# Kernel tuning notes

Hardware: AMD Instinct MI355X
Metric: run time of the kernel (lower is better)

## Reference

```python
import jax, jax.numpy as jnp
import numpy as np

BIN_SIZE = 500      # bin_size from __init__
K = 5               # num_neighbors
DIST_MULT = 0.1
MAX_NUM_BINS = 200


def setup_inputs() -> dict:
    key = jax.random.key(0)
    k1, k2 = jax.random.split(key)
    points = jax.random.normal(k1, (2, 5000, 64), dtype=jnp.float32)
    # codebook_random_rotations: [n_features, max_num_bins // 2]
    rotations = jax.random.normal(k2, (64, MAX_NUM_BINS // 2), dtype=jnp.float32)
    return {"points": points, "rotations": rotations}


def reference(points, rotations):
    """Dense equivalent of the batched tf.SparseTensor output [B, N, N].

    tf.sparse.add sums duplicate (src, dst) entries, which scatter-add
    reproduces exactly.
    """
    B, N, F = points.shape
    nbins = N // BIN_SIZE

    # LSH projection: use first nbins//2 rotation columns, mirror with -mul.
    mul = jnp.einsum('bnf,fh->bnh', points, rotations[:, : nbins // 2])
    cmul = jnp.concatenate([mul, -mul], axis=-1)          # [B, N, nbins]
    bin_idx = jnp.argmax(cmul, axis=-1)                   # [B, N]
    # split_indices_to_bins: stable argsort of bin assignment, reshape to bins
    bins_split = jnp.argsort(bin_idx, axis=-1, stable=True).reshape(B, nbins, BIN_SIZE)

    # gather points into bins: [B, nbins, BIN_SIZE, F]
    parts = jnp.take_along_axis(points, bins_split.reshape(B, N, 1), axis=1)
    parts = parts.reshape(B, nbins, BIN_SIZE, F)

    # pairwise_dist within each bin
    na = jnp.sum(parts * parts, axis=-1)                  # [B, nbins, bs]
    gram = jnp.einsum('bgif,bgjf->bgij', parts, parts)    # [B, nbins, bs, bs]
    dm = jnp.sqrt(jnp.maximum(na[..., :, None] - 2.0 * gram + na[..., None, :], 1e-6))
    aff = jnp.exp(-DIST_MULT * dm)                        # [B, nbins, bs, bs]

    # top-k neighbors per point within its bin
    vals, idx = jax.lax.top_k(aff, K)                     # [B, nbins, bs, K]

    # map local bin indices back to global point indices
    dst = jax.vmap(jax.vmap(lambda b, i: b[i]))(bins_split, idx)   # [B, nbins, bs, K]
    src = jnp.broadcast_to(bins_split[..., None], dst.shape)
    b_ix = jnp.broadcast_to(jnp.arange(B)[:, None, None, None], dst.shape)

    # scatter-add (duplicates summed, as in repeated tf.sparse.add)
    out = jnp.zeros((B, N, N), dtype=points.dtype)
    out = out.at[b_ix, src, dst].add(vals)
    return out
```

## Files before the change

### kernel.cpp

```cpp
#include <hip/hip_runtime.h>
#include <cfloat>
#include <cstddef>

#define NBATCH 2
#define NPTS   5000
#define NF     64
#define NB     10
#define BINSZ  500
#define TOPK   5
#define ROTCOLS 100

#define NCB    8
#define CBS    64
#define NCAND  (NCB * TOPK)
#define NCOMP  (NBATCH * NB * NCB)
#define NZERO  1888
#define OUT4   (NBATCH * NPTS * NPTS / 4)

__global__ __launch_bounds__(256) void bin_norm_k(const float* __restrict__ pts,
                                                  const float* __restrict__ rot,
                                                  int* __restrict__ bin_idx,
                                                  float* __restrict__ na) {
    __shared__ float srot[NF * 5];
    const int t = threadIdx.x;
    for (int i = t; i < NF * 5; i += 256) {
        int f = i / 5, h = i - 5 * f;
        srot[i] = rot[f * ROTCOLS + h];
    }
    __syncthreads();

    int pt   = blockIdx.x * 4 + (t >> 6);
    int lane = t & 63;
    float p  = pts[(size_t)pt * NF + lane];
    float nn = p * p;
    float c0 = p * srot[lane * 5 + 0];
    float c1 = p * srot[lane * 5 + 1];
    float c2 = p * srot[lane * 5 + 2];
    float c3 = p * srot[lane * 5 + 3];
    float c4 = p * srot[lane * 5 + 4];
    #pragma unroll
    for (int off = 32; off > 0; off >>= 1) {
        nn += __shfl_xor(nn, off);
        c0 += __shfl_xor(c0, off);
        c1 += __shfl_xor(c1, off);
        c2 += __shfl_xor(c2, off);
        c3 += __shfl_xor(c3, off);
        c4 += __shfl_xor(c4, off);
    }
    if (lane == 0) {
        float c[5] = {c0, c1, c2, c3, c4};
        float bv = c[0]; int bi = 0;
        #pragma unroll
        for (int h = 1; h < 5; ++h) if (c[h] > bv) { bv = c[h]; bi = h; }
        #pragma unroll
        for (int h = 0; h < 5; ++h) if (-c[h] > bv) { bv = -c[h]; bi = h + 5; }
        bin_idx[pt] = bi;
        na[pt] = nn;
    }
}

__global__ __launch_bounds__(256) void sort_k(const int* __restrict__ bin_idx,
                                              int* __restrict__ order) {
    const int b = blockIdx.x;
    const int t = threadIdx.x;
    const int w = t >> 6, lane = t & 63;
    __shared__ int sh_bin[NPTS];
    __shared__ int sh_hist[256][NB];
    __shared__ int sh_part[NB][16];
    __shared__ int sh_tot[NB + 1];

    for (int i = t; i < NPTS; i += 256) sh_bin[i] = bin_idx[b * NPTS + i];
    #pragma unroll
    for (int h = 0; h < NB; ++h) sh_hist[t][h] = 0;
    __syncthreads();

    const int CH = (NPTS + 255) / 256;
    const int i0 = t * CH;
    const int i1 = (i0 + CH < NPTS) ? (i0 + CH) : NPTS;
    for (int i = i0; i < i1; ++i) sh_hist[t][sh_bin[i]]++;
    __syncthreads();

    if (t < NB * 16) {
        int h = t >> 4, s = t & 15;
        int sum = 0;
        #pragma unroll
        for (int k = 0; k < 16; ++k) sum += sh_hist[s * 16 + k][h];
        sh_part[h][s] = sum;
    }
    __syncthreads();
    if (t < NB) {
        int tot = 0;
        #pragma unroll
        for (int s = 0; s < 16; ++s) tot += sh_part[t][s];
        sh_tot[t + 1] = tot;
    }
    __syncthreads();
    if (t == 0) {
        sh_tot[0] = 0;
        for (int h = 1; h <= NB; ++h) sh_tot[h] += sh_tot[h - 1];
    }
    __syncthreads();

    for (int h = w; h < NB; h += 4) {
        int base = lane * 4;
        int v0 = sh_hist[base + 0][h];
        int v1 = sh_hist[base + 1][h];
        int v2 = sh_hist[base + 2][h];
        int v3 = sh_hist[base + 3][h];
        int lt = v0 + v1 + v2 + v3;
        int x = lt;
        #pragma unroll
        for (int off = 1; off < 64; off <<= 1) {
            int y = __shfl_up(x, off);
            if (lane >= off) x += y;
        }
        int excl = x - lt + sh_tot[h];
        sh_hist[base + 0][h] = excl;
        sh_hist[base + 1][h] = excl + v0;
        sh_hist[base + 2][h] = excl + v0 + v1;
        sh_hist[base + 3][h] = excl + v0 + v1 + v2;
    }
    __syncthreads();

    for (int i = i0; i < i1; ++i) {
        int h = sh_bin[i];
        order[b * NPTS + sh_hist[t][h]++] = i;
    }
}

__global__ __launch_bounds__(256) void pair_zero_k(const float* __restrict__ pts,
                                                   const float* __restrict__ na,
                                                   const int* __restrict__ order,
                                                   float* __restrict__ wv,
                                                   int* __restrict__ wd,
                                                   float* __restrict__ out) {
    const int bx  = blockIdx.x;
    const int tid = threadIdx.x;

    if (bx >= NCOMP) {
        const int z = bx - NCOMP;
        const int chunk = (OUT4 + NZERO - 1) / NZERO;
        const size_t base = (size_t)z * chunk;
        size_t end = base + chunk; if (end > (size_t)OUT4) end = OUT4;
        float4* o4 = (float4*)out;
        const float4 z4 = make_float4(0.f, 0.f, 0.f, 0.f);
        for (size_t i = base + tid; i < end; i += 256) o4[i] = z4;
        return;
    }

    const int g   = bx / NCB;
    const int cb  = bx - g * NCB;
    const int b   = g / NB;
    const int grp = g - b * NB;
    const int c0  = cb * CBS;
    const int ncols = (c0 + CBS <= BINSZ) ? CBS : (BINSZ - c0);

    __shared__ float sh_cols[CBS * NF];
    __shared__ float sh_cna[CBS];

    const int* ord = order + b * NPTS + grp * BINSZ;
    const float4* p4 = (const float4*)(pts + (size_t)b * NPTS * NF);
    float4* sc4 = (float4*)sh_cols;

    for (int i = tid; i < ncols * 16; i += 256) {
        int c = i >> 4, q = i & 15;
        sc4[c * 16 + q] = p4[(size_t)ord[c0 + c] * 16 + q];
    }
    if (tid < ncols) sh_cna[tid] = na[b * NPTS + ord[c0 + tid]];
    __syncthreads();

    const int p0 = tid, p1 = tid + 256;
    const bool h1 = (p1 < BINSZ);
    const int gi0 = ord[p0];
    const int gi1 = h1 ? ord[p1] : gi0;
    float4 r0[16], r1[16];
    #pragma unroll
    for (int q = 0; q < 16; ++q) {
        r0[q] = p4[(size_t)gi0 * 16 + q];
        r1[q] = p4[(size_t)gi1 * 16 + q];
    }
    const float na0 = na[b * NPTS + gi0];
    const float na1 = na[b * NPTS + gi1];

    float tv0[TOPK], tv1[TOPK]; int tp0[TOPK], tp1[TOPK];
    #pragma unroll
    for (int s = 0; s < TOPK; ++s) { tv0[s] = FLT_MAX; tv1[s] = FLT_MAX; tp0[s] = 0; tp1[s] = 0; }

    for (int c = 0; c < ncols; ++c) {
        const float4* cq = sc4 + c * 16;
        float a0 = 0.f, a1 = 0.f;
        #pragma unroll
        for (int q = 0; q < 16; ++q) {
            float4 cc = cq[q];
            a0 += r0[q].x * cc.x; a0 += r0[q].y * cc.y;
            a0 += r0[q].z * cc.z; a0 += r0[q].w * cc.w;
            a1 += r1[q].x * cc.x; a1 += r1[q].y * cc.y;
            a1 += r1[q].z * cc.z; a1 += r1[q].w * cc.w;
        }
        const float cna = sh_cna[c];
        const int pos = c0 + c;
        float d0 = na0 - 2.f * a0 + cna;
        float d1 = na1 - 2.f * a1 + cna;
        if (d0 < tv0[TOPK - 1]) {
            tv0[TOPK - 1] = d0; tp0[TOPK - 1] = pos;
            #pragma unroll
            for (int s = TOPK - 1; s > 0; --s) {
                if (tv0[s] < tv0[s - 1]) {
                    float fv = tv0[s]; tv0[s] = tv0[s - 1]; tv0[s - 1] = fv;
                    int   fi = tp0[s]; tp0[s] = tp0[s - 1]; tp0[s - 1] = fi;
                }
            }
        }
        if (h1 && d1 < tv1[TOPK - 1]) {
            tv1[TOPK - 1] = d1; tp1[TOPK - 1] = pos;
            #pragma unroll
            for (int s = TOPK - 1; s > 0; --s) {
                if (tv1[s] < tv1[s - 1]) {
                    float fv = tv1[s]; tv1[s] = tv1[s - 1]; tv1[s - 1] = fv;
                    int   fi = tp1[s]; tp1[s] = tp1[s - 1]; tp1[s - 1] = fi;
                }
            }
        }
    }

    const int slotbase = (b * NB + grp) * BINSZ;
    {
        size_t wbase = ((size_t)(slotbase + p0) * NCB + cb) * TOPK;
        #pragma unroll
        for (int s = 0; s < TOPK; ++s) { wv[wbase + s] = tv0[s]; wd[wbase + s] = tp0[s]; }
    }
    if (h1) {
        size_t wbase = ((size_t)(slotbase + p1) * NCB + cb) * TOPK;
        #pragma unroll
        for (int s = 0; s < TOPK; ++s) { wv[wbase + s] = tv1[s]; wd[wbase + s] = tp1[s]; }
    }
}

__global__ __launch_bounds__(256) void merge_inject_k(const float* __restrict__ wv,
                                                      const int* __restrict__ wd,
                                                      const int* __restrict__ order,
                                                      float* __restrict__ out) {
    const int slot = blockIdx.x * 256 + threadIdx.x;
    if (slot >= NBATCH * NPTS) return;
    const int b   = slot / (NB * BINSZ);
    const int rem = slot - b * NB * BINSZ;
    const int grp = rem / BINSZ;
    const int p   = rem - grp * BINSZ;
    const int* ord = order + b * NPTS + grp * BINSZ;
    const int src = ord[p];

    float cv[NCAND]; int cp[NCAND];
    const size_t base = (size_t)slot * NCAND;
    #pragma unroll
    for (int k = 0; k < NCAND; ++k) { cv[k] = wv[base + k]; cp[k] = wd[base + k]; }

    unsigned long long used = 0;
    float* orow = out + ((size_t)b * NPTS + src) * NPTS;
    #pragma unroll
    for (int s = 0; s < TOPK; ++s) {
        float bv = FLT_MAX; int bp = 0x7fffffff; int bk = 0;
        #pragma unroll
        for (int k = 0; k < NCAND; ++k) {
            bool ok = !((used >> k) & 1ull);
            bool better = ok && ((cv[k] < bv) || (cv[k] == bv && cp[k] < bp));
            if (better) { bv = cv[k]; bp = cp[k]; bk = k; }
        }
        used |= (1ull << bk);
        float val = expf(-0.1f * sqrtf(fmaxf(bv, 1e-6f)));
        orow[ord[bp]] = val;
    }
}

extern "C" void kernel_launch(void* const* d_in, const int* in_sizes, int n_in,
                              void* d_out, int out_size, void* d_ws, size_t ws_size,
                              hipStream_t stream) {
    const float* points = (const float*)d_in[0];
    const float* rot    = (const float*)d_in[1];
    float* out = (float*)d_out;

    char* ws = (char*)d_ws;
    int*   bin_idx = (int*)ws;   ws += NBATCH * NPTS * sizeof(int);
    float* na      = (float*)ws; ws += NBATCH * NPTS * sizeof(float);
    int*   order   = (int*)ws;   ws += NBATCH * NPTS * sizeof(int);
    float* wv      = (float*)ws; ws += (size_t)NBATCH * NPTS * NCAND * sizeof(float);
    int*   wd      = (int*)ws;

    bin_norm_k<<<(NBATCH * NPTS) / 4, 256, 0, stream>>>(points, rot, bin_idx, na);
    sort_k<<<NBATCH, 256, 0, stream>>>(bin_idx, order);
    pair_zero_k<<<NCOMP + NZERO, 256, 0, stream>>>(points, na, order, wv, wd, out);
    merge_inject_k<<<(NBATCH * NPTS + 255) / 256, 256, 0, stream>>>(wv, wd, order, out);
}
```

Measured before the change: 92.02 us.

## Stream bin columns from global memory and merge candidates with insertion top-k

The pairwise kernel no longer stages a 64-column tile in shared memory. Each block now handles a 50-column slice, and every thread reads each column's feature vector directly from global memory. Because the column address is the same across the wave, the compiler may turn these reads into scalar or broadcast loads and skip the barrier. Rows are remapped so each 64-lane wave covers two row groups 64 apart. The merge kernel replaces five selection passes over all candidates with a single streaming insertion pass using the same tie-break, which cuts register arrays and repeated scans. Splitting into 10 column slices raises the candidate count per point from 40 to 50, so the workspace grows and the merge has more entries to read.

Result: slower. 107.2 us (+16.5%).

```diff
diff --git a/kernel.cpp b/kernel.cpp
--- a/kernel.cpp
+++ b/kernel.cpp
@@ -10,11 +10,11 @@
 #define TOPK   5
 #define ROTCOLS 100
 
-#define NCB    8
-#define CBS    64
-#define NCAND  (NCB * TOPK)
-#define NCOMP  (NBATCH * NB * NCB)
-#define NZERO  1888
+#define NCS    10
+#define CSW    50
+#define NCAND  (NCS * TOPK)
+#define NCOMPB (NBATCH * NB * NCS)
+#define NZB    1800
 #define OUT4   (NBATCH * NPTS * NPTS / 4)
 
 __global__ __launch_bounds__(256) void bin_norm_k(const float* __restrict__ pts,
@@ -137,9 +137,9 @@
     const int bx  = blockIdx.x;
     const int tid = threadIdx.x;
 
-    if (bx >= NCOMP) {
-        const int z = bx - NCOMP;
-        const int chunk = (OUT4 + NZERO - 1) / NZERO;
+    if (bx >= NCOMPB) {
+        const int z = bx - NCOMPB;
+        const int chunk = (OUT4 + NZB - 1) / NZB;
         const size_t base = (size_t)z * chunk;
         size_t end = base + chunk; if (end > (size_t)OUT4) end = OUT4;
         float4* o4 = (float4*)out;
@@ -148,28 +148,20 @@
         return;
     }
 
-    const int g   = bx / NCB;
-    const int cb  = bx - g * NCB;
-    const int b   = g / NB;
-    const int grp = g - b * NB;
-    const int c0  = cb * CBS;
-    const int ncols = (c0 + CBS <= BINSZ) ? CBS : (BINSZ - c0);
-
-    __shared__ float sh_cols[CBS * NF];
-    __shared__ float sh_cna[CBS];
+    const int g    = bx / NCS;
+    const int cs   = bx - g * NCS;
+    const int b    = g / NB;
+    const int grp  = g - b * NB;
+    const int rs   = tid >> 6;
+    const int lane = tid & 63;
+    const int c0   = cs * CSW;
 
     const int* ord = order + b * NPTS + grp * BINSZ;
     const float4* p4 = (const float4*)(pts + (size_t)b * NPTS * NF);
-    float4* sc4 = (float4*)sh_cols;
-
-    for (int i = tid; i < ncols * 16; i += 256) {
-        int c = i >> 4, q = i & 15;
-        sc4[c * 16 + q] = p4[(size_t)ord[c0 + c] * 16 + q];
-    }
-    if (tid < ncols) sh_cna[tid] = na[b * NPTS + ord[c0 + tid]];
-    __syncthreads();
-
-    const int p0 = tid, p1 = tid + 256;
+    const float* nab = na + b * NPTS;
+
+    const int p0 = rs * 128 + lane;
+    const int p1 = p0 + 64;
     const bool h1 = (p1 < BINSZ);
     const int gi0 = ord[p0];
     const int gi1 = h1 ? ord[p1] : gi0;
@@ -179,26 +171,29 @@
         r0[q] = p4[(size_t)gi0 * 16 + q];
         r1[q] = p4[(size_t)gi1 * 16 + q];
     }
-    const float na0 = na[b * NPTS + gi0];
-    const float na1 = na[b * NPTS + gi1];
+    const float na0 = nab[gi0];
+    const float na1 = nab[gi1];
 
     float tv0[TOPK], tv1[TOPK]; int tp0[TOPK], tp1[TOPK];
     #pragma unroll
     for (int s = 0; s < TOPK; ++s) { tv0[s] = FLT_MAX; tv1[s] = FLT_MAX; tp0[s] = 0; tp1[s] = 0; }
 
-    for (int c = 0; c < ncols; ++c) {
-        const float4* cq = sc4 + c * 16;
+    for (int c = 0; c < CSW; ++c) {
+        const int pos = c0 + c;
+        const int gj = ord[pos];
+        const float4* cp = p4 + (size_t)gj * 16;
+        const float cna = nab[gj];
+        float4 cc[16];
+        #pragma unroll
+        for (int q = 0; q < 16; ++q) cc[q] = cp[q];
         float a0 = 0.f, a1 = 0.f;
         #pragma unroll
         for (int q = 0; q < 16; ++q) {
-            float4 cc = cq[q];
-            a0 += r0[q].x * cc.x; a0 += r0[q].y * cc.y;
-            a0 += r0[q].z * cc.z; a0 += r0[q].w * cc.w;
-            a1 += r1[q].x * cc.x; a1 += r1[q].y * cc.y;
-            a1 += r1[q].z * cc.z; a1 += r1[q].w * cc.w;
-        }
-        const float cna = sh_cna[c];
-        const int pos = c0 + c;
+            a0 += r0[q].x * cc[q].x; a0 += r0[q].y * cc[q].y;
+            a0 += r0[q].z * cc[q].z; a0 += r0[q].w * cc[q].w;
+            a1 += r1[q].x * cc[q].x; a1 += r1[q].y * cc[q].y;
+            a1 += r1[q].z * cc[q].z; a1 += r1[q].w * cc[q].w;
+        }
         float d0 = na0 - 2.f * a0 + cna;
         float d1 = na1 - 2.f * a1 + cna;
         if (d0 < tv0[TOPK - 1]) {
@@ -225,12 +220,12 @@
 
     const int slotbase = (b * NB + grp) * BINSZ;
     {
-        size_t wbase = ((size_t)(slotbase + p0) * NCB + cb) * TOPK;
+        size_t wbase = ((size_t)(slotbase + p0) * NCS + cs) * TOPK;
         #pragma unroll
         for (int s = 0; s < TOPK; ++s) { wv[wbase + s] = tv0[s]; wd[wbase + s] = tp0[s]; }
     }
     if (h1) {
-        size_t wbase = ((size_t)(slotbase + p1) * NCB + cb) * TOPK;
+        size_t wbase = ((size_t)(slotbase + p1) * NCS + cs) * TOPK;
         #pragma unroll
         for (int s = 0; s < TOPK; ++s) { wv[wbase + s] = tv1[s]; wd[wbase + s] = tp1[s]; }
     }
@@ -249,25 +244,33 @@
     const int* ord = order + b * NPTS + grp * BINSZ;
     const int src = ord[p];
 
-    float cv[NCAND]; int cp[NCAND];
+    float tv[TOPK]; int tp[TOPK];
+    #pragma unroll
+    for (int s = 0; s < TOPK; ++s) { tv[s] = FLT_MAX; tp[s] = 0x7fffffff; }
+
     const size_t base = (size_t)slot * NCAND;
-    #pragma unroll
-    for (int k = 0; k < NCAND; ++k) { cv[k] = wv[base + k]; cp[k] = wd[base + k]; }
-
-    unsigned long long used = 0;
+    for (int k = 0; k < NCAND; ++k) {
+        float v = wv[base + k];
+        int   q = wd[base + k];
+        bool ins = (v < tv[TOPK - 1]) || (v == tv[TOPK - 1] && q < tp[TOPK - 1]);
+        if (ins) {
+            tv[TOPK - 1] = v; tp[TOPK - 1] = q;
+            #pragma unroll
+            for (int s = TOPK - 1; s > 0; --s) {
+                bool sw = (tv[s] < tv[s - 1]) || (tv[s] == tv[s - 1] && tp[s] < tp[s - 1]);
+                if (sw) {
+                    float fv = tv[s]; tv[s] = tv[s - 1]; tv[s - 1] = fv;
+                    int   fi = tp[s]; tp[s] = tp[s - 1]; tp[s - 1] = fi;
+                }
+            }
+        }
+    }
+
     float* orow = out + ((size_t)b * NPTS + src) * NPTS;
     #pragma unroll
     for (int s = 0; s < TOPK; ++s) {
-        float bv = FLT_MAX; int bp = 0x7fffffff; int bk = 0;
-        #pragma unroll
-        for (int k = 0; k < NCAND; ++k) {
-            bool ok = !((used >> k) & 1ull);
-            bool better = ok && ((cv[k] < bv) || (cv[k] == bv && cp[k] < bp));
-            if (better) { bv = cv[k]; bp = cp[k]; bk = k; }
-        }
-        used |= (1ull << bk);
-        float val = expf(-0.1f * sqrtf(fmaxf(bv, 1e-6f)));
-        orow[ord[bp]] = val;
+        float val = expf(-0.1f * sqrtf(fmaxf(tv[s], 1e-6f)));
+        orow[ord[tp[s]]] = val;
     }
 }
 
@@ -287,6 +290,6 @@
 
     bin_norm_k<<<(NBATCH * NPTS) / 4, 256, 0, stream>>>(points, rot, bin_idx, na);
     sort_k<<<NBATCH, 256, 0, stream>>>(bin_idx, order);
-    pair_zero_k<<<NCOMP + NZERO, 256, 0, stream>>>(points, na, order, wv, wd, out);
+    pair_zero_k<<<NCOMPB + NZB, 256, 0, stream>>>(points, na, order, wv, wd, out);
     merge_inject_k<<<(NBATCH * NPTS + 255) / 256, 256, 0, stream>>>(wv, wd, order, out);
 }
```

## Spread output zeroing across all four kernels and fuse tail rows into merge

Applied to the files above, without the earlier changes.

The 200 MB dense output zero-fill is split into row ranges: the first kernels zero rows 0-999 and 1000-1799 alongside binning and sorting, the pair kernel zeroes rows up to 7800, and the merge kernel zeroes the last rows itself before injecting top-k values. Stores switch to nontemporal for most ranges. An inverse permutation is added so merge indexes by output row, letting each block own whole rows and write its values after its own zeroing. The aim is to hide the bandwidth-bound memset behind the otherwise latency-bound small kernels. The cost is that merge now uses only 4 active threads per block for the top-k work, and correctness depends on the ordering of zeroing against the injected writes across kernels.

Result: slower. 114.9 us (+24.8%).

```diff
diff --git a/kernel.cpp b/kernel.cpp
--- a/kernel.cpp
+++ b/kernel.cpp
@@ -13,16 +13,45 @@
 #define NCB    8
 #define CBS    64
 #define NCAND  (NCB * TOPK)
-#define NCOMP  (NBATCH * NB * NCB)
-#define NZERO  1888
+#define ROW4   (NPTS / 4)
 #define OUT4   (NBATCH * NPTS * NPTS / 4)
 
-__global__ __launch_bounds__(256) void bin_norm_k(const float* __restrict__ pts,
-                                                  const float* __restrict__ rot,
-                                                  int* __restrict__ bin_idx,
-                                                  float* __restrict__ na) {
+#define Z1_BEG 0
+#define Z1_END (1000 * ROW4)
+#define Z2_END (1800 * ROW4)
+#define Z3_END (7800 * ROW4)
+#define NZ1    400
+#define NZ2    300
+#define NZ3    1800
+#define ROWCUT 7800
+
+typedef float nfloat4 __attribute__((ext_vector_type(4)));
+
+__device__ __forceinline__ void nt_zero4(float4* p) {
+    nfloat4 z = {0.f, 0.f, 0.f, 0.f};
+    __builtin_nontemporal_store(z, (nfloat4*)p);
+}
+
+__device__ __forceinline__ void zero_range(float4* o4, size_t beg, size_t end,
+                                           int nblk, int zid, int tid) {
+    const size_t total = end - beg;
+    const size_t chunk = (total + nblk - 1) / nblk;
+    size_t lo = beg + (size_t)zid * chunk;
+    size_t hi = lo + chunk; if (hi > end) hi = end;
+    for (size_t i = lo + tid; i < hi; i += 256) nt_zero4(o4 + i);
+}
+
+__global__ __launch_bounds__(256) void bin_norm_zero_k(const float* __restrict__ pts,
+                                                       const float* __restrict__ rot,
+                                                       int* __restrict__ bin_idx,
+                                                       float* __restrict__ na,
+                                                       float* __restrict__ out) {
+    const int t = threadIdx.x;
+    if (blockIdx.x >= 2500) {
+        zero_range((float4*)out, Z1_BEG, Z1_END, NZ1, blockIdx.x - 2500, t);
+        return;
+    }
     __shared__ float srot[NF * 5];
-    const int t = threadIdx.x;
     for (int i = t; i < NF * 5; i += 256) {
         int f = i / 5, h = i - 5 * f;
         srot[i] = rot[f * ROTCOLS + h];
@@ -59,10 +88,16 @@
     }
 }
 
-__global__ __launch_bounds__(256) void sort_k(const int* __restrict__ bin_idx,
-                                              int* __restrict__ order) {
+__global__ __launch_bounds__(256) void sort_zero_k(const int* __restrict__ bin_idx,
+                                                   int* __restrict__ order,
+                                                   int* __restrict__ inv,
+                                                   float* __restrict__ out) {
+    const int t = threadIdx.x;
+    if (blockIdx.x >= NBATCH) {
+        zero_range((float4*)out, Z1_END, Z2_END, NZ2, blockIdx.x - NBATCH, t);
+        return;
+    }
     const int b = blockIdx.x;
-    const int t = threadIdx.x;
     const int w = t >> 6, lane = t & 63;
     __shared__ int sh_bin[NPTS];
     __shared__ int sh_hist[256][NB];
@@ -124,7 +159,9 @@
 
     for (int i = i0; i < i1; ++i) {
         int h = sh_bin[i];
-        order[b * NPTS + sh_hist[t][h]++] = i;
+        int sp = sh_hist[t][h]++;
+        order[b * NPTS + sp] = i;
+        inv[b * NPTS + i] = sp;
     }
 }
 
@@ -137,14 +174,8 @@
     const int bx  = blockIdx.x;
     const int tid = threadIdx.x;
 
-    if (bx >= NCOMP) {
-        const int z = bx - NCOMP;
-        const int chunk = (OUT4 + NZERO - 1) / NZERO;
-        const size_t base = (size_t)z * chunk;
-        size_t end = base + chunk; if (end > (size_t)OUT4) end = OUT4;
-        float4* o4 = (float4*)out;
-        const float4 z4 = make_float4(0.f, 0.f, 0.f, 0.f);
-        for (size_t i = base + tid; i < end; i += 256) o4[i] = z4;
+    if (bx >= NBATCH * NB * NCB) {
+        zero_range((float4*)out, Z2_END, Z3_END, NZ3, bx - NBATCH * NB * NCB, tid);
         return;
     }
 
@@ -239,35 +270,43 @@
 __global__ __launch_bounds__(256) void merge_inject_k(const float* __restrict__ wv,
                                                       const int* __restrict__ wd,
                                                       const int* __restrict__ order,
+                                                      const int* __restrict__ inv,
                                                       float* __restrict__ out) {
-    const int slot = blockIdx.x * 256 + threadIdx.x;
-    if (slot >= NBATCH * NPTS) return;
-    const int b   = slot / (NB * BINSZ);
-    const int rem = slot - b * NB * BINSZ;
-    const int grp = rem / BINSZ;
-    const int p   = rem - grp * BINSZ;
-    const int* ord = order + b * NPTS + grp * BINSZ;
-    const int src = ord[p];
-
-    float cv[NCAND]; int cp[NCAND];
-    const size_t base = (size_t)slot * NCAND;
-    #pragma unroll
-    for (int k = 0; k < NCAND; ++k) { cv[k] = wv[base + k]; cp[k] = wd[base + k]; }
-
-    unsigned long long used = 0;
-    float* orow = out + ((size_t)b * NPTS + src) * NPTS;
-    #pragma unroll
-    for (int s = 0; s < TOPK; ++s) {
-        float bv = FLT_MAX; int bp = 0x7fffffff; int bk = 0;
-        #pragma unroll
-        for (int k = 0; k < NCAND; ++k) {
-            bool ok = !((used >> k) & 1ull);
-            bool better = ok && ((cv[k] < bv) || (cv[k] == bv && cp[k] < bp));
-            if (better) { bv = cv[k]; bp = cp[k]; bk = k; }
-        }
-        used |= (1ull << bk);
-        float val = expf(-0.1f * sqrtf(fmaxf(bv, 1e-6f)));
-        orow[ord[bp]] = val;
+    const int t = threadIdx.x;
+    const size_t gr0 = (size_t)blockIdx.x * 4;
+    if (gr0 >= ROWCUT) {
+        float4* o4 = ((float4*)out) + gr0 * ROW4;
+        const float4 z4 = make_float4(0.f, 0.f, 0.f, 0.f);
+        for (int i = t; i < 4 * ROW4; i += 256) o4[i] = z4;
+        __syncthreads();
+    }
+    if (t < 4) {
+        const size_t g = gr0 + t;
+        const int b  = (int)(g / NPTS);
+        const int sp = inv[g];
+        const int grp = sp / BINSZ;
+
+        float cv[NCAND]; int cp[NCAND];
+        const size_t base = ((size_t)b * NPTS + sp) * NCAND;
+        #pragma unroll
+        for (int k = 0; k < NCAND; ++k) { cv[k] = wv[base + k]; cp[k] = wd[base + k]; }
+
+        const int* ord = order + b * NPTS + grp * BINSZ;
+        unsigned long long used = 0;
+        float* orow = out + g * NPTS;
+        #pragma unroll
+        for (int s = 0; s < TOPK; ++s) {
+            float bv = FLT_MAX; int bp = 0x7fffffff; int bk = 0;
+            #pragma unroll
+            for (int k = 0; k < NCAND; ++k) {
+                bool ok = !((used >> k) & 1ull);
+                bool better = ok && ((cv[k] < bv) || (cv[k] == bv && cp[k] < bp));
+                if (better) { bv = cv[k]; bp = cp[k]; bk = k; }
+            }
+            used |= (1ull << bk);
+            float val = expf(-0.1f * sqrtf(fmaxf(bv, 1e-6f)));
+            orow[ord[bp]] = val;
+        }
     }
 }
 
@@ -282,11 +321,12 @@
     int*   bin_idx = (int*)ws;   ws += NBATCH * NPTS * sizeof(int);
     float* na      = (float*)ws; ws += NBATCH * NPTS * sizeof(float);
     int*   order   = (int*)ws;   ws += NBATCH * NPTS * sizeof(int);
+    int*   inv     = (int*)ws;   ws += NBATCH * NPTS * sizeof(int);
     float* wv      = (float*)ws; ws += (size_t)NBATCH * NPTS * NCAND * sizeof(float);
     int*   wd      = (int*)ws;
 
-    bin_norm_k<<<(NBATCH * NPTS) / 4, 256, 0, stream>>>(points, rot, bin_idx, na);
-    sort_k<<<NBATCH, 256, 0, stream>>>(bin_idx, order);
-    pair_zero_k<<<NCOMP + NZERO, 256, 0, stream>>>(points, na, order, wv, wd, out);
-    merge_inject_k<<<(NBATCH * NPTS + 255) / 256, 256, 0, stream>>>(wv, wd, order, out);
-}
+    bin_norm_zero_k<<<2500 + NZ1, 256, 0, stream>>>(points, rot, bin_idx, na, out);
+    sort_zero_k<<<NBATCH + NZ2, 256, 0, stream>>>(bin_idx, order, inv, out);
+    pair_zero_k<<<NBATCH * NB * NCB + NZ3, 256, 0, stream>>>(points, na, order, wv, wd, out);
+    merge_inject_k<<<(NBATCH * NPTS) / 4, 256, 0, stream>>>(wv, wd, order, inv, out);
+}
```

## Fuse all stages into one cooperative persistent kernel with grid syncs

Applied to the files above, without the earlier changes.

Replaces the four separate launches (bin/norm, sort, pairwise top-k plus zeroing, merge/inject) with a single cooperative kernel of 256 blocks that separates phases with grid-wide syncs. Output zeroing now runs in the first phase alongside binning, and shared memory is reused through a union across phases. This removes launch gaps between kernels, but each phase now runs on only 256 blocks, so the 200MB zero fill and the compute spread less widely, and grid syncs add their own cost. Unused fallback kernels (one with an empty body) are left behind.

Result: slower. 211.2 us (+129.5%).

```diff
diff --git a/kernel.cpp b/kernel.cpp
--- a/kernel.cpp
+++ b/kernel.cpp
@@ -1,6 +1,9 @@
 #include <hip/hip_runtime.h>
+#include <hip/hip_cooperative_groups.h>
 #include <cfloat>
 #include <cstddef>
+
+namespace cg = cooperative_groups;
 
 #define NBATCH 2
 #define NPTS   5000
@@ -13,262 +16,277 @@
 #define NCB    8
 #define CBS    64
 #define NCAND  (NCB * TOPK)
-#define NCOMP  (NBATCH * NB * NCB)
-#define NZERO  1888
 #define OUT4   (NBATCH * NPTS * NPTS / 4)
-
-__global__ __launch_bounds__(256) void bin_norm_k(const float* __restrict__ pts,
+#define GRID   256
+
+union SMem {
+    float srot[NF * 5];
+    struct { int bin[NPTS]; int hist[256][NB]; int part[NB][16]; int tot[NB + 1]; } so;
+    struct { float cols[CBS * NF]; float cna[CBS]; } pa;
+};
+
+__global__ __launch_bounds__(256, 2) void fused_k(const float* __restrict__ pts,
                                                   const float* __restrict__ rot,
+                                                  float* __restrict__ na,
                                                   int* __restrict__ bin_idx,
-                                                  float* __restrict__ na) {
-    __shared__ float srot[NF * 5];
-    const int t = threadIdx.x;
+                                                  int* __restrict__ order,
+                                                  float* __restrict__ wv,
+                                                  int* __restrict__ wd,
+                                                  float* __restrict__ out) {
+    cg::grid_group gg = cg::this_grid();
+    __shared__ SMem sm;
+    const int bx = blockIdx.x;
+    const int t  = threadIdx.x;
+
     for (int i = t; i < NF * 5; i += 256) {
         int f = i / 5, h = i - 5 * f;
-        srot[i] = rot[f * ROTCOLS + h];
+        sm.srot[i] = rot[f * ROTCOLS + h];
     }
     __syncthreads();
-
-    int pt   = blockIdx.x * 4 + (t >> 6);
-    int lane = t & 63;
-    float p  = pts[(size_t)pt * NF + lane];
-    float nn = p * p;
-    float c0 = p * srot[lane * 5 + 0];
-    float c1 = p * srot[lane * 5 + 1];
-    float c2 = p * srot[lane * 5 + 2];
-    float c3 = p * srot[lane * 5 + 3];
-    float c4 = p * srot[lane * 5 + 4];
-    #pragma unroll
-    for (int off = 32; off > 0; off >>= 1) {
-        nn += __shfl_xor(nn, off);
-        c0 += __shfl_xor(c0, off);
-        c1 += __shfl_xor(c1, off);
-        c2 += __shfl_xor(c2, off);
-        c3 += __shfl_xor(c3, off);
-        c4 += __shfl_xor(c4, off);
-    }
-    if (lane == 0) {
-        float c[5] = {c0, c1, c2, c3, c4};
-        float bv = c[0]; int bi = 0;
-        #pragma unroll
-        for (int h = 1; h < 5; ++h) if (c[h] > bv) { bv = c[h]; bi = h; }
-        #pragma unroll
-        for (int h = 0; h < 5; ++h) if (-c[h] > bv) { bv = -c[h]; bi = h + 5; }
-        bin_idx[pt] = bi;
-        na[pt] = nn;
-    }
-}
-
-__global__ __launch_bounds__(256) void sort_k(const int* __restrict__ bin_idx,
-                                              int* __restrict__ order) {
-    const int b = blockIdx.x;
-    const int t = threadIdx.x;
-    const int w = t >> 6, lane = t & 63;
-    __shared__ int sh_bin[NPTS];
-    __shared__ int sh_hist[256][NB];
-    __shared__ int sh_part[NB][16];
-    __shared__ int sh_tot[NB + 1];
-
-    for (int i = t; i < NPTS; i += 256) sh_bin[i] = bin_idx[b * NPTS + i];
-    #pragma unroll
-    for (int h = 0; h < NB; ++h) sh_hist[t][h] = 0;
-    __syncthreads();
-
-    const int CH = (NPTS + 255) / 256;
-    const int i0 = t * CH;
-    const int i1 = (i0 + CH < NPTS) ? (i0 + CH) : NPTS;
-    for (int i = i0; i < i1; ++i) sh_hist[t][sh_bin[i]]++;
-    __syncthreads();
-
-    if (t < NB * 16) {
-        int h = t >> 4, s = t & 15;
-        int sum = 0;
-        #pragma unroll
-        for (int k = 0; k < 16; ++k) sum += sh_hist[s * 16 + k][h];
-        sh_part[h][s] = sum;
-    }
-    __syncthreads();
-    if (t < NB) {
-        int tot = 0;
-        #pragma unroll
-        for (int s = 0; s < 16; ++s) tot += sh_part[t][s];
-        sh_tot[t + 1] = tot;
-    }
-    __syncthreads();
-    if (t == 0) {
-        sh_tot[0] = 0;
-        for (int h = 1; h <= NB; ++h) sh_tot[h] += sh_tot[h - 1];
-    }
-    __syncthreads();
-
-    for (int h = w; h < NB; h += 4) {
-        int base = lane * 4;
-        int v0 = sh_hist[base + 0][h];
-        int v1 = sh_hist[base + 1][h];
-        int v2 = sh_hist[base + 2][h];
-        int v3 = sh_hist[base + 3][h];
-        int lt = v0 + v1 + v2 + v3;
-        int x = lt;
-        #pragma unroll
-        for (int off = 1; off < 64; off <<= 1) {
-            int y = __shfl_up(x, off);
-            if (lane >= off) x += y;
-        }
-        int excl = x - lt + sh_tot[h];
-        sh_hist[base + 0][h] = excl;
-        sh_hist[base + 1][h] = excl + v0;
-        sh_hist[base + 2][h] = excl + v0 + v1;
-        sh_hist[base + 3][h] = excl + v0 + v1 + v2;
-    }
-    __syncthreads();
-
-    for (int i = i0; i < i1; ++i) {
-        int h = sh_bin[i];
-        order[b * NPTS + sh_hist[t][h]++] = i;
-    }
-}
-
-__global__ __launch_bounds__(256) void pair_zero_k(const float* __restrict__ pts,
-                                                   const float* __restrict__ na,
-                                                   const int* __restrict__ order,
-                                                   float* __restrict__ wv,
-                                                   int* __restrict__ wd,
-                                                   float* __restrict__ out) {
-    const int bx  = blockIdx.x;
-    const int tid = threadIdx.x;
-
-    if (bx >= NCOMP) {
-        const int z = bx - NCOMP;
-        const int chunk = (OUT4 + NZERO - 1) / NZERO;
-        const size_t base = (size_t)z * chunk;
-        size_t end = base + chunk; if (end > (size_t)OUT4) end = OUT4;
+    for (int rnd = 0; rnd < 10; ++rnd) {
+        int pt = bx * 40 + rnd * 4 + (t >> 6);
+        if (pt < NBATCH * NPTS) {
+            int lane = t & 63;
+            float p  = pts[(size_t)pt * NF + lane];
+            float nn = p * p;
+            float c0 = p * sm.srot[lane * 5 + 0];
+            float c1 = p * sm.srot[lane * 5 + 1];
+            float c2 = p * sm.srot[lane * 5 + 2];
+            float c3 = p * sm.srot[lane * 5 + 3];
+            float c4 = p * sm.srot[lane * 5 + 4];
+            #pragma unroll
+            for (int off = 32; off > 0; off >>= 1) {
+                nn += __shfl_xor(nn, off);
+                c0 += __shfl_xor(c0, off);
+                c1 += __shfl_xor(c1, off);
+                c2 += __shfl_xor(c2, off);
+                c3 += __shfl_xor(c3, off);
+                c4 += __shfl_xor(c4, off);
+            }
+            if (lane == 0) {
+                float c[5] = {c0, c1, c2, c3, c4};
+                float bv = c[0]; int bi = 0;
+                #pragma unroll
+                for (int h = 1; h < 5; ++h) if (c[h] > bv) { bv = c[h]; bi = h; }
+                #pragma unroll
+                for (int h = 0; h < 5; ++h) if (-c[h] > bv) { bv = -c[h]; bi = h + 5; }
+                bin_idx[pt] = bi;
+                na[pt] = nn;
+            }
+        }
+    }
+
+    {
+        const int chunk = (OUT4 + GRID - 1) / GRID;
+        size_t lo = (size_t)bx * chunk;
+        size_t hi = lo + chunk; if (hi > (size_t)OUT4) hi = OUT4;
         float4* o4 = (float4*)out;
         const float4 z4 = make_float4(0.f, 0.f, 0.f, 0.f);
-        for (size_t i = base + tid; i < end; i += 256) o4[i] = z4;
-        return;
-    }
-
-    const int g   = bx / NCB;
-    const int cb  = bx - g * NCB;
-    const int b   = g / NB;
-    const int grp = g - b * NB;
-    const int c0  = cb * CBS;
-    const int ncols = (c0 + CBS <= BINSZ) ? CBS : (BINSZ - c0);
-
-    __shared__ float sh_cols[CBS * NF];
-    __shared__ float sh_cna[CBS];
-
-    const int* ord = order + b * NPTS + grp * BINSZ;
-    const float4* p4 = (const float4*)(pts + (size_t)b * NPTS * NF);
-    float4* sc4 = (float4*)sh_cols;
-
-    for (int i = tid; i < ncols * 16; i += 256) {
-        int c = i >> 4, q = i & 15;
-        sc4[c * 16 + q] = p4[(size_t)ord[c0 + c] * 16 + q];
-    }
-    if (tid < ncols) sh_cna[tid] = na[b * NPTS + ord[c0 + tid]];
-    __syncthreads();
-
-    const int p0 = tid, p1 = tid + 256;
-    const bool h1 = (p1 < BINSZ);
-    const int gi0 = ord[p0];
-    const int gi1 = h1 ? ord[p1] : gi0;
-    float4 r0[16], r1[16];
-    #pragma unroll
-    for (int q = 0; q < 16; ++q) {
-        r0[q] = p4[(size_t)gi0 * 16 + q];
-        r1[q] = p4[(size_t)gi1 * 16 + q];
-    }
-    const float na0 = na[b * NPTS + gi0];
-    const float na1 = na[b * NPTS + gi1];
-
-    float tv0[TOPK], tv1[TOPK]; int tp0[TOPK], tp1[TOPK];
-    #pragma unroll
-    for (int s = 0; s < TOPK; ++s) { tv0[s] = FLT_MAX; tv1[s] = FLT_MAX; tp0[s] = 0; tp1[s] = 0; }
-
-    for (int c = 0; c < ncols; ++c) {
-        const float4* cq = sc4 + c * 16;
-        float a0 = 0.f, a1 = 0.f;
+        for (size_t i = lo + t; i < hi; i += 256) o4[i] = z4;
+    }
+    gg.sync();
+
+    if (bx < NBATCH) {
+        const int b = bx;
+        const int w = t >> 6, lane = t & 63;
+        for (int i = t; i < NPTS; i += 256) sm.so.bin[i] = bin_idx[b * NPTS + i];
+        #pragma unroll
+        for (int h = 0; h < NB; ++h) sm.so.hist[t][h] = 0;
+        __syncthreads();
+
+        const int CH = (NPTS + 255) / 256;
+        const int i0 = t * CH;
+        const int i1 = (i0 + CH < NPTS) ? (i0 + CH) : NPTS;
+        for (int i = i0; i < i1; ++i) sm.so.hist[t][sm.so.bin[i]]++;
+        __syncthreads();
+
+        if (t < NB * 16) {
+            int h = t >> 4, s = t & 15;
+            int sum = 0;
+            #pragma unroll
+            for (int k = 0; k < 16; ++k) sum += sm.so.hist[s * 16 + k][h];
+            sm.so.part[h][s] = sum;
+        }
+        __syncthreads();
+        if (t < NB) {
+            int tot = 0;
+            #pragma unroll
+            for (int s = 0; s < 16; ++s) tot += sm.so.part[t][s];
+            sm.so.tot[t + 1] = tot;
+        }
+        __syncthreads();
+        if (t == 0) {
+            sm.so.tot[0] = 0;
+            for (int h = 1; h <= NB; ++h) sm.so.tot[h] += sm.so.tot[h - 1];
+        }
+        __syncthreads();
+
+        for (int h = w; h < NB; h += 4) {
+            int base = lane * 4;
+            int v0 = sm.so.hist[base + 0][h];
+            int v1 = sm.so.hist[base + 1][h];
+            int v2 = sm.so.hist[base + 2][h];
+            int v3 = sm.so.hist[base + 3][h];
+            int lt = v0 + v1 + v2 + v3;
+            int x = lt;
+            #pragma unroll
+            for (int off = 1; off < 64; off <<= 1) {
+                int y = __shfl_up(x, off);
+                if (lane >= off) x += y;
+            }
+            int excl = x - lt + sm.so.tot[h];
+            sm.so.hist[base + 0][h] = excl;
+            sm.so.hist[base + 1][h] = excl + v0;
+            sm.so.hist[base + 2][h] = excl + v0 + v1;
+            sm.so.hist[base + 3][h] = excl + v0 + v1 + v2;
+        }
+        __syncthreads();
+
+        for (int i = i0; i < i1; ++i) {
+            int h = sm.so.bin[i];
+            order[b * NPTS + sm.so.hist[t][h]++] = i;
+        }
+    }
+    gg.sync();
+
+    if (bx < NBATCH * NB * NCB) {
+        const int g   = bx / NCB;
+        const int cb  = bx - g * NCB;
+        const int b   = g / NB;
+        const int grp = g - b * NB;
+        const int c0  = cb * CBS;
+        const int ncols = (c0 + CBS <= BINSZ) ? CBS : (BINSZ - c0);
+
+        const int* ord = order + b * NPTS + grp * BINSZ;
+        const float4* p4 = (const float4*)(pts + (size_t)b * NPTS * NF);
+        float4* sc4 = (float4*)sm.pa.cols;
+
+        for (int i = t; i < ncols * 16; i += 256) {
+            int c = i >> 4, q = i & 15;
+            sc4[c * 16 + q] = p4[(size_t)ord[c0 + c] * 16 + q];
+        }
+        if (t < ncols) sm.pa.cna[t] = na[b * NPTS + ord[c0 + t]];
+        __syncthreads();
+
+        const int p0 = t, p1 = t + 256;
+        const bool h1 = (p1 < BINSZ);
+        const int gi0 = ord[p0];
+        const int gi1 = h1 ? ord[p1] : gi0;
+        float4 r0[16], r1[16];
         #pragma unroll
         for (int q = 0; q < 16; ++q) {
-            float4 cc = cq[q];
-            a0 += r0[q].x * cc.x; a0 += r0[q].y * cc.y;
-            a0 += r0[q].z * cc.z; a0 += r0[q].w * cc.w;
-            a1 += r1[q].x * cc.x; a1 += r1[q].y * cc.y;
-            a1 += r1[q].z * cc.z; a1 += r1[q].w * cc.w;
-        }
-        const float cna = sh_cna[c];
-        const int pos = c0 + c;
-        float d0 = na0 - 2.f * a0 + cna;
-        float d1 = na1 - 2.f * a1 + cna;
-        if (d0 < tv0[TOPK - 1]) {
-            tv0[TOPK - 1] = d0; tp0[TOPK - 1] = pos;
-            #pragma unroll
-            for (int s = TOPK - 1; s > 0; --s) {
-                if (tv0[s] < tv0[s - 1]) {
-                    float fv = tv0[s]; tv0[s] = tv0[s - 1]; tv0[s - 1] = fv;
-                    int   fi = tp0[s]; tp0[s] = tp0[s - 1]; tp0[s - 1] = fi;
+            r0[q] = p4[(size_t)gi0 * 16 + q];
+            r1[q] = p4[(size_t)gi1 * 16 + q];
+        }
+        const float na0 = na[b * NPTS + gi0];
+        const float na1 = na[b * NPTS + gi1];
+
+        float tv0[TOPK], tv1[TOPK]; int tp0[TOPK], tp1[TOPK];
+        #pragma unroll
+        for (int s = 0; s < TOPK; ++s) { tv0[s] = FLT_MAX; tv1[s] = FLT_MAX; tp0[s] = 0; tp1[s] = 0; }
+
+        for (int c = 0; c < ncols; ++c) {
+            const float4* cq = sc4 + c * 16;
+            float a0 = 0.f, a1 = 0.f;
+            #pragma unroll
+            for (int q = 0; q < 16; ++q) {
+                float4 cc = cq[q];
+                a0 += r0[q].x * cc.x; a0 += r0[q].y * cc.y;
+                a0 += r0[q].z * cc.z; a0 += r0[q].w * cc.w;
+                a1 += r1[q].x * cc.x; a1 += r1[q].y * cc.y;
+                a1 += r1[q].z * cc.z; a1 += r1[q].w * cc.w;
+            }
+            const float cna = sm.pa.cna[c];
+            const int pos = c0 + c;
+            float d0 = na0 - 2.f * a0 + cna;
+            float d1 = na1 - 2.f * a1 + cna;
+            if (d0 < tv0[TOPK - 1]) {
+                tv0[TOPK - 1] = d0; tp0[TOPK - 1] = pos;
+                #pragma unroll
+                for (int s = TOPK - 1; s > 0; --s) {
+                    if (tv0[s] < tv0[s - 1]) {
+                        float fv = tv0[s]; tv0[s] = tv0[s - 1]; tv0[s - 1] = fv;
+                        int   fi = tp0[s]; tp0[s] = tp0[s - 1]; tp0[s - 1] = fi;
+                    }
                 }
             }
-        }
-        if (h1 && d1 < tv1[TOPK - 1]) {
-            tv1[TOPK - 1] = d1; tp1[TOPK - 1] = pos;
-            #pragma unroll
-            for (int s = TOPK - 1; s > 0; --s) {
-                if (tv1[s] < tv1[s - 1]) {
-                    float fv = tv1[s]; tv1[s] = tv1[s - 1]; tv1[s - 1] = fv;
-                    int   fi = tp1[s]; tp1[s] = tp1[s - 1]; tp1[s - 1] = fi;
+            if (h1 && d1 < tv1[TOPK - 1]) {
+                tv1[TOPK - 1] = d1; tp1[TOPK - 1] = pos;
+                #pragma unroll
+                for (int s = TOPK - 1; s > 0; --s) {
+                    if (tv1[s] < tv1[s - 1]) {
+                        float fv = tv1[s]; tv1[s] = tv1[s - 1]; tv1[s - 1] = fv;
+                        int   fi = tp1[s]; tp1[s] = tp1[s - 1]; tp1[s - 1] = fi;
+                    }
                 }
             }
         }
-    }
-
-    const int slotbase = (b * NB + grp) * BINSZ;
+
+        const int slotbase = (b * NB + grp) * BINSZ;
+        {
+            size_t wbase = ((size_t)(slotbase + p0) * NCB + cb) * TOPK;
+            #pragma unroll
+            for (int s = 0; s < TOPK; ++s) { wv[wbase + s] = tv0[s]; wd[wbase + s] = tp0[s]; }
+        }
+        if (h1) {
+            size_t wbase = ((size_t)(slotbase + p1) * NCB + cb) * TOPK;
+            #pragma unroll
+            for (int s = 0; s < TOPK; ++s) { wv[wbase + s] = tv1[s]; wd[wbase + s] = tp1[s]; }
+        }
+    }
+    gg.sync();
+
     {
-        size_t wbase = ((size_t)(slotbase + p0) * NCB + cb) * TOPK;
-        #pragma unroll
-        for (int s = 0; s < TOPK; ++s) { wv[wbase + s] = tv0[s]; wd[wbase + s] = tp0[s]; }
-    }
-    if (h1) {
-        size_t wbase = ((size_t)(slotbase + p1) * NCB + cb) * TOPK;
-        #pragma unroll
-        for (int s = 0; s < TOPK; ++s) { wv[wbase + s] = tv1[s]; wd[wbase + s] = tp1[s]; }
+        const int slot = bx * 256 + t;
+        if (slot < NBATCH * NPTS) {
+            const int b   = slot / (NB * BINSZ);
+            const int rem = slot - b * NB * BINSZ;
+            const int grp = rem / BINSZ;
+            const int p   = rem - grp * BINSZ;
+            const int* ord = order + b * NPTS + grp * BINSZ;
+            const int src = ord[p];
+
+            float cv[NCAND]; int cp[NCAND];
+            const size_t base = (size_t)slot * NCAND;
+            #pragma unroll
+            for (int k = 0; k < NCAND; ++k) { cv[k] = wv[base + k]; cp[k] = wd[base + k]; }
+
+            unsigned long long used = 0;
+            float* orow = out + ((size_t)b * NPTS + src) * NPTS;
+            #pragma unroll
+            for (int s = 0; s < TOPK; ++s) {
+                float bv = FLT_MAX; int bp = 0x7fffffff; int bk = 0;
+                #pragma unroll
+                for (int k = 0; k < NCAND; ++k) {
+                    bool ok = !((used >> k) & 1ull);
+                    bool better = ok && ((cv[k] < bv) || (cv[k] == bv && cp[k] < bp));
+                    if (better) { bv = cv[k]; bp = cp[k]; bk = k; }
+                }
+                used |= (1ull << bk);
+                float val = expf(-0.1f * sqrtf(fmaxf(bv, 1e-6f)));
+                orow[ord[bp]] = val;
+            }
+        }
     }
 }
 
-__global__ __launch_bounds__(256) void merge_inject_k(const float* __restrict__ wv,
-                                                      const int* __restrict__ wd,
-                                                      const int* __restrict__ order,
-                                                      float* __restrict__ out) {
-    const int slot = blockIdx.x * 256 + threadIdx.x;
-    if (slot >= NBATCH * NPTS) return;
-    const int b   = slot / (NB * BINSZ);
-    const int rem = slot - b * NB * BINSZ;
-    const int grp = rem / BINSZ;
-    const int p   = rem - grp * BINSZ;
-    const int* ord = order + b * NPTS + grp * BINSZ;
-    const int src = ord[p];
-
-    float cv[NCAND]; int cp[NCAND];
-    const size_t base = (size_t)slot * NCAND;
-    #pragma unroll
-    for (int k = 0; k < NCAND; ++k) { cv[k] = wv[base + k]; cp[k] = wd[base + k]; }
-
-    unsigned long long used = 0;
-    float* orow = out + ((size_t)b * NPTS + src) * NPTS;
-    #pragma unroll
-    for (int s = 0; s < TOPK; ++s) {
-        float bv = FLT_MAX; int bp = 0x7fffffff; int bk = 0;
-        #pragma unroll
-        for (int k = 0; k < NCAND; ++k) {
-            bool ok = !((used >> k) & 1ull);
-            bool better = ok && ((cv[k] < bv) || (cv[k] == bv && cp[k] < bp));
-            if (better) { bv = cv[k]; bp = cp[k]; bk = k; }
-        }
-        used |= (1ull << bk);
-        float val = expf(-0.1f * sqrtf(fmaxf(bv, 1e-6f)));
-        orow[ord[bp]] = val;
-    }
+__global__ __launch_bounds__(256) void fb_zero_k(float* __restrict__ out) {
+    const int chunk = (OUT4 + 2047) / 2048;
+    size_t lo = (size_t)blockIdx.x * chunk;
+    size_t hi = lo + chunk; if (hi > (size_t)OUT4) hi = OUT4;
+    float4* o4 = (float4*)out;
+    const float4 z4 = make_float4(0.f, 0.f, 0.f, 0.f);
+    for (size_t i = lo + threadIdx.x; i < hi; i += 256) o4[i] = z4;
+}
+__global__ __launch_bounds__(256) void fb_all_k(const float* __restrict__ pts,
+                                                const float* __restrict__ rot,
+                                                float* __restrict__ na,
+                                                int* __restrict__ bin_idx,
+                                                int* __restrict__ order,
+                                                float* __restrict__ wv,
+                                                int* __restrict__ wd,
+                                                float* __restrict__ out,
+                                                const int* __restrict__ phase) {
 }
 
 extern "C" void kernel_launch(void* const* d_in, const int* in_sizes, int n_in,
@@ -279,14 +297,14 @@
     float* out = (float*)d_out;
 
     char* ws = (char*)d_ws;
+    float* na      = (float*)ws; ws += NBATCH * NPTS * sizeof(float);
     int*   bin_idx = (int*)ws;   ws += NBATCH * NPTS * sizeof(int);
-    float* na      = (float*)ws; ws += NBATCH * NPTS * sizeof(float);
     int*   order   = (int*)ws;   ws += NBATCH * NPTS * sizeof(int);
     float* wv      = (float*)ws; ws += (size_t)NBATCH * NPTS * NCAND * sizeof(float);
     int*   wd      = (int*)ws;
 
-    bin_norm_k<<<(NBATCH * NPTS) / 4, 256, 0, stream>>>(points, rot, bin_idx, na);
-    sort_k<<<NBATCH, 256, 0, stream>>>(bin_idx, order);
-    pair_zero_k<<<NCOMP + NZERO, 256, 0, stream>>>(points, na, order, wv, wd, out);
-    merge_inject_k<<<(NBATCH * NPTS + 255) / 256, 256, 0, stream>>>(wv, wd, order, out);
+    void* args[] = {(void*)&points, (void*)&rot, (void*)&na, (void*)&bin_idx,
+                    (void*)&order, (void*)&wv, (void*)&wd, (void*)&out};
+    hipLaunchCooperativeKernel((const void*)fused_k, dim3(GRID), dim3(256),
+                               args, 0, stream);
 }
```
